# Performance work log

Measured on AMD Instinct MI355X. Metric: run time of the kernel, lower is better.

Reference implementation:

```python
import jax, jax.numpy as jnp
import numpy as np

N_NODES = 100000
N_EDGES = 800000
N_ETYPES = 5
IN_DIM = 23
HID_DIM = 128
OUT_DIM = 64
NUM_GRAPHS = 64


def setup_inputs() -> dict:
    key = jax.random.key(0)
    ks = jax.random.split(key, 8)
    feat = jax.random.normal(ks[0], (N_NODES, IN_DIM), dtype=jnp.float32)
    src = jax.random.randint(ks[1], (N_ETYPES, N_EDGES), 0, N_NODES, dtype=jnp.int32)
    dst = jax.random.randint(ks[2], (N_ETYPES, N_EDGES), 0, N_NODES, dtype=jnp.int32)
    graph_ids = jnp.sort(jax.random.randint(ks[3], (N_NODES,), 0, NUM_GRAPHS, dtype=jnp.int32))
    W1 = jax.random.normal(ks[4], (N_ETYPES, IN_DIM, HID_DIM), dtype=jnp.float32) * 0.1
    b1 = jnp.zeros((N_ETYPES, HID_DIM), dtype=jnp.float32)
    W2 = jax.random.normal(ks[5], (N_ETYPES, HID_DIM, OUT_DIM), dtype=jnp.float32) * 0.1
    b2 = jnp.zeros((N_ETYPES, OUT_DIM), dtype=jnp.float32)
    return {"feat": feat, "src": src, "dst": dst, "graph_ids": graph_ids,
            "W1": W1, "b1": b1, "W2": W2, "b2": b2}


def _hetero_sage_layer(h, src, dst, W, b):
    """HeteroGraphConv of SAGEConv(aggregator='gcn') summed over edge types.
    gcn aggregator: h_neigh[i] = (sum_{j->i} h[j] + h[i]) / (in_deg(i) + 1);
    per-etype output = h_neigh @ W_e + b_e; combine with sum."""
    n = h.shape[0]
    out = jnp.zeros((n, W.shape[-1]), dtype=h.dtype)
    ones_e = jnp.ones((src.shape[1],), dtype=h.dtype)
    for e in range(N_ETYPES):
        deg = jax.ops.segment_sum(ones_e, dst[e], num_segments=n)          # [N]
        agg = jax.ops.segment_sum(h[src[e]], dst[e], num_segments=n)       # [N, D]
        h_neigh = (agg + h) / (deg + 1.0)[:, None]
        out = out + h_neigh @ W[e] + b[e]
    return out


def reference(feat, src, dst, graph_ids, W1, b1, W2, b2):
    # layer 1: in_dim -> hid, relu (dropout in eval mode = identity)
    h = jax.nn.relu(_hetero_sage_layer(feat, src, dst, W1, b1))
    # layer 2: hid -> out (no activation)
    h = _hetero_sage_layer(h, src, dst, W2, b2)
    # dgl.mean_nodes: per-graph mean over nodes
    counts = jax.ops.segment_sum(jnp.ones((h.shape[0],), h.dtype), graph_ids,
                                 num_segments=NUM_GRAPHS)
    sums = jax.ops.segment_sum(h, graph_ids, num_segments=NUM_GRAPHS)
    return sums / jnp.maximum(counts, 1.0)[:, None]
```

## Files before the change

kernel.cpp:

```cpp
#include <hip/hip_runtime.h>

#define N_NODES   100000
#define N_EDGES   800000
#define N_ETYPES  5
#define IN_DIM    23
#define FPAD      32
#define HID_DIM   128
#define OUT_DIM   64
#define NUM_GRAPHS 64
#define NBKT      391
#define PBLK      125
#define CHUNK     6400
#define PN        (N_ETYPES*NBKT*PBLK)
#define SCAN_NBLK ((PN + 1023) / 1024)
#define TOT_EDGES (N_ETYPES*N_EDGES)
#define BKT_CAP   3072
#define ASTR      136
#define A1STR     40


__device__ __forceinline__ unsigned short f2bf(float x) {
    unsigned u = __float_as_uint(x);
    unsigned r = (u + 0x7FFFu + ((u >> 16) & 1u)) >> 16;
    return (unsigned short)r;
}
__device__ __forceinline__ float bf2f(unsigned short h) {
    return __uint_as_float(((unsigned)h) << 16);
}

typedef __attribute__((ext_vector_type(8))) short bf16x8;
typedef __attribute__((ext_vector_type(4))) float f32x4;
typedef __attribute__((ext_vector_type(2))) float f32x2;

__global__ __launch_bounds__(256) void cvt_feat_k(const float* __restrict__ feat,
                                                  unsigned short* __restrict__ fb32) {
    int i = blockIdx.x * 256 + threadIdx.x;
    if (i < N_NODES * FPAD) {
        int n = i >> 5, d = i & 31;
        fb32[i] = (d < IN_DIM) ? f2bf(feat[n * IN_DIM + d]) : (unsigned short)0;
    }
}

__global__ __launch_bounds__(256) void cvt_w2t_k(const float* __restrict__ W2,
                                                 unsigned short* __restrict__ w2tb) {
    int i = blockIdx.x * 256 + threadIdx.x;
    if (i < N_ETYPES * OUT_DIM * HID_DIM) {
        int e = i / (OUT_DIM * HID_DIM);
        int r = i - e * (OUT_DIM * HID_DIM);
        int n = r >> 7, k = r & 127;
        w2tb[i] = f2bf(W2[(e * HID_DIM + k) * OUT_DIM + n]);
    }
}

__global__ __launch_bounds__(256) void cvt_w1t_k(const float* __restrict__ W1,
                                                 unsigned short* __restrict__ w1tb) {
    int i = blockIdx.x * 256 + threadIdx.x;
    if (i < N_ETYPES * HID_DIM * 32) {
        int e = i / (HID_DIM * 32);
        int r = i - e * (HID_DIM * 32);
        int n = r >> 5, k = r & 31;
        w1tb[i] = (k < IN_DIM) ? f2bf(W1[e * IN_DIM * HID_DIM + k * HID_DIM + n])
                               : (unsigned short)0;
    }
}

__global__ __launch_bounds__(128) void cvt_b1s_k(const float* __restrict__ b1,
                                                 float* __restrict__ b1s) {
    int d = threadIdx.x;
    float s = 0.f;
    for (int e = 0; e < N_ETYPES; e++) s += b1[e * HID_DIM + d];
    b1s[d] = s;
}

__global__ __launch_bounds__(256) void part1_k(const int* __restrict__ dst,
                                               int* __restrict__ hp) {
    __shared__ int hist[NBKT];
    int e = blockIdx.y, blk = blockIdx.x, t = threadIdx.x;
    for (int b = t; b < NBKT; b += 256) hist[b] = 0;
    __syncthreads();
    const int* dp = dst + e * N_EDGES + blk * CHUNK;
    for (int k = t; k < CHUNK; k += 256) atomicAdd(&hist[dp[k] >> 8], 1);
    __syncthreads();
    for (int b = t; b < NBKT; b += 256) hp[(e * NBKT + b) * PBLK + blk] = hist[b];
}

__global__ __launch_bounds__(256) void scan1_k(const int* __restrict__ in,
                                               int* __restrict__ out,
                                               int* __restrict__ bsum) {
    __shared__ int ls[256];
    int t = threadIdx.x;
    int base = blockIdx.x * 1024 + t * 4;
    int v[4]; int s = 0;
    for (int j = 0; j < 4; j++) { int i = base + j; v[j] = (i < PN) ? in[i] : 0; s += v[j]; }
    ls[t] = s; __syncthreads();
    for (int o = 1; o < 256; o <<= 1) {
        int x = (t >= o) ? ls[t - o] : 0;
        __syncthreads();
        ls[t] += x;
        __syncthreads();
    }
    int run = (t > 0) ? ls[t - 1] : 0;
    if (t == 255) bsum[blockIdx.x] = ls[255];
    for (int j = 0; j < 4; j++) { int i = base + j; if (i < PN) out[i] = run; run += v[j]; }
}

__global__ __launch_bounds__(256) void scan2_k(int* __restrict__ bsum) {
    __shared__ int ls[256];
    int t = threadIdx.x;
    int v = (t < SCAN_NBLK) ? bsum[t] : 0;
    ls[t] = v; __syncthreads();
    for (int o = 1; o < 256; o <<= 1) {
        int x = (t >= o) ? ls[t - o] : 0;
        __syncthreads();
        ls[t] += x;
        __syncthreads();
    }
    if (t < SCAN_NBLK) bsum[t] = (t > 0) ? ls[t - 1] : 0;
}

__global__ __launch_bounds__(256) void scan3_k(int* __restrict__ off,
                                               const int* __restrict__ bsum) {
    int i = blockIdx.x * 256 + threadIdx.x;
    if (i < PN) off[i] += bsum[i >> 10];
}

__global__ __launch_bounds__(256) void part2_k(const int* __restrict__ src,
                                               const int* __restrict__ dst,
                                               const int* __restrict__ off,
                                               unsigned* __restrict__ ep) {
    __shared__ int cur[NBKT];
    int e = blockIdx.y, blk = blockIdx.x, t = threadIdx.x;
    for (int b = t; b < NBKT; b += 256) cur[b] = off[(e * NBKT + b) * PBLK + blk];
    __syncthreads();
    const int* dp = dst + e * N_EDGES + blk * CHUNK;
    const int* sp = src + e * N_EDGES + blk * CHUNK;
    for (int k = t; k < CHUNK; k += 256) {
        int d = dp[k], s = sp[k];
        int b = d >> 8;
        int pos = atomicAdd(&cur[b], 1);
        ep[pos] = (unsigned)s | ((unsigned)(d & 255) << 24);
    }
}

__global__ __launch_bounds__(256) void sort_k(const int* __restrict__ off,
                                              const unsigned* __restrict__ ep,
                                              unsigned* __restrict__ csr,
                                              int* __restrict__ noff,
                                              int* __restrict__ degn,
                                              float* __restrict__ inv) {
    __shared__ unsigned recs[BKT_CAP];
    __shared__ int hist[256];
    __shared__ int scn[256];
    __shared__ int curp[256];
    int b = blockIdx.x, e = blockIdx.y, t = threadIdx.x;
    int lin = (e * NBKT + b) * PBLK;
    int S = off[lin];
    int E = (lin == PN - PBLK) ? TOT_EDGES : off[lin + PBLK];
    int cnt = E - S;
    hist[t] = 0;
    __syncthreads();
    for (int i = t; i < cnt; i += 256) {
        unsigned r = ep[S + i];
        recs[i] = r;
        atomicAdd(&hist[r >> 24], 1);
    }
    __syncthreads();
    scn[t] = hist[t];
    __syncthreads();
    for (int o = 1; o < 256; o <<= 1) {
        int x = (t >= o) ? scn[t - o] : 0;
        __syncthreads();
        scn[t] += x;
        __syncthreads();
    }
    int excl = scn[t] - hist[t];
    curp[t] = excl;
    int n = b * 256 + t;
    if (n < N_NODES) {
        noff[e * N_NODES + n] = S + excl;
        degn[e * N_NODES + n] = hist[t];
        inv[e * N_NODES + n]  = 1.f / (float)(hist[t] + 1);
    }
    __syncthreads();
    for (int i = t; i < cnt; i += 256) {
        unsigned r = recs[i];
        int pos = atomicAdd(&curp[r >> 24], 1);
        csr[S + pos] = r & 0xFFFFFFu;
    }
}

__global__ __launch_bounds__(256) void agg1_k(const int* __restrict__ noff,
                                              const int* __restrict__ degn,
                                              const unsigned* __restrict__ csr,
                                              const unsigned short* __restrict__ fb32,
                                              const float* __restrict__ inv,
                                              unsigned short* __restrict__ agg1b) {
    int e = blockIdx.y;
    int t = threadIdx.x;
    int lane = t & 15;
    int n = blockIdx.x * 16 + (t >> 4);
    int idx = e * N_NODES + n;
    int st = noff[idx];
    int cnt = degn[idx];
    ushort2 sv = *(const ushort2*)&fb32[n * FPAD + lane * 2];
    float a0 = bf2f(sv.x), a1 = bf2f(sv.y);
    int k = 0;
    for (; k + 3 < cnt; k += 4) {
        int s0 = csr[st + k];
        int s1 = csr[st + k + 1];
        int s2 = csr[st + k + 2];
        int s3 = csr[st + k + 3];
        ushort2 v0 = *(const ushort2*)&fb32[s0 * FPAD + lane * 2];
        ushort2 v1 = *(const ushort2*)&fb32[s1 * FPAD + lane * 2];
        ushort2 v2 = *(const ushort2*)&fb32[s2 * FPAD + lane * 2];
        ushort2 v3 = *(const ushort2*)&fb32[s3 * FPAD + lane * 2];
        a0 += bf2f(v0.x) + bf2f(v1.x) + bf2f(v2.x) + bf2f(v3.x);
        a1 += bf2f(v0.y) + bf2f(v1.y) + bf2f(v2.y) + bf2f(v3.y);
    }
    for (; k < cnt; k++) {
        int s0 = csr[st + k];
        ushort2 v0 = *(const ushort2*)&fb32[s0 * FPAD + lane * 2];
        a0 += bf2f(v0.x);
        a1 += bf2f(v0.y);
    }
    float iv = inv[idx];
    ushort2 o; o.x = f2bf(a0 * iv); o.y = f2bf(a1 * iv);
    *(ushort2*)&agg1b[(size_t)idx * 32 + lane * 2] = o;
}

__global__ __launch_bounds__(256) void gemm1_k(const unsigned short* __restrict__ agg1b,
                                               const unsigned short* __restrict__ w1tb,
                                               const float* __restrict__ b1s,
                                               unsigned short* __restrict__ h1b) {
    __shared__ unsigned short As[64 * A1STR];
    __shared__ unsigned short Wt[128 * A1STR];
    int t = threadIdx.x;
    int node0 = blockIdx.x * 64;
    int w = t >> 6, lane = t & 63;
    int m = lane & 15, quad = lane >> 4;

    f32x4 acc[8];
    for (int nt = 0; nt < 8; nt++) {
        float bb = b1s[nt * 16 + m];
        f32x4 c = {bb, bb, bb, bb};
        acc[nt] = c;
    }

    for (int e = 0; e < N_ETYPES; e++) {
        __syncthreads();
        for (int j = t; j < 64 * 8; j += 256) {
            int n = j >> 3, c4 = (j & 7) * 4;
            int gn = node0 + n;
            int cn = gn < N_NODES ? gn : N_NODES - 1;
            *(ushort4*)&As[n * A1STR + c4] =
                *(const ushort4*)&agg1b[(size_t)(e * N_NODES + cn) * 32 + c4];
        }
        for (int j = t; j < 128 * 8; j += 256) {
            int n = j >> 3, c4 = (j & 7) * 4;
            *(ushort4*)&Wt[n * A1STR + c4] =
                *(const ushort4*)&w1tb[(size_t)(e * HID_DIM + n) * 32 + c4];
        }
        __syncthreads();
        bf16x8 a = *(const bf16x8*)&As[(w * 16 + m) * A1STR + quad * 8];
        for (int nt = 0; nt < 8; nt++) {
            bf16x8 b = *(const bf16x8*)&Wt[(nt * 16 + m) * A1STR + quad * 8];
            acc[nt] = __builtin_amdgcn_mfma_f32_16x16x32_bf16(a, b, acc[nt], 0, 0, 0);
        }
    }
    for (int nt = 0; nt < 8; nt++) {
        for (int r = 0; r < 4; r++) {
            int gn = node0 + w * 16 + quad * 4 + r;
            if (gn < N_NODES)
                h1b[(size_t)gn * HID_DIM + nt * 16 + m] = f2bf(fmaxf(acc[nt][r], 0.f));
        }
    }
}

__global__ __launch_bounds__(256) void gemm2_k(const unsigned short* __restrict__ h1b,
                                               const unsigned short* __restrict__ w2tb,
                                               unsigned char* __restrict__ t2f8) {
    __shared__ unsigned short As[64 * ASTR];
    __shared__ unsigned short Wt[64 * ASTR];
    int t = threadIdx.x;
    int node0 = blockIdx.x * 64;
    int w = t >> 6, lane = t & 63;
    int m = lane & 15, quad = lane >> 4;

    for (int j = t; j < 64 * 32; j += 256) {
        int n = j >> 5, c4 = (j & 31) * 4;
        int gn = node0 + n;
        int cn = gn < N_NODES ? gn : N_NODES - 1;
        *(ushort4*)&As[n * ASTR + c4] = *(const ushort4*)&h1b[cn * HID_DIM + c4];
    }
    __syncthreads();
    bf16x8 a[4];
    for (int ks = 0; ks < 4; ks++)
        a[ks] = *(const bf16x8*)&As[(w * 16 + m) * ASTR + ks * 32 + quad * 8];

    for (int e = 0; e < N_ETYPES; e++) {
        __syncthreads();
        for (int j = t; j < 64 * 32; j += 256) {
            int n = j >> 5, c4 = (j & 31) * 4;
            *(ushort4*)&Wt[n * ASTR + c4] =
                *(const ushort4*)&w2tb[(e * OUT_DIM + n) * HID_DIM + c4];
        }
        __syncthreads();
        unsigned char* out = t2f8 + (size_t)e * N_NODES * OUT_DIM;
        for (int nt = 0; nt < 4; nt++) {
            f32x4 c = {0.f, 0.f, 0.f, 0.f};
            for (int ks = 0; ks < 4; ks++) {
                bf16x8 b = *(const bf16x8*)&Wt[(nt * 16 + m) * ASTR + ks * 32 + quad * 8];
                c = __builtin_amdgcn_mfma_f32_16x16x32_bf16(a[ks], b, c, 0, 0, 0);
            }
            for (int r = 0; r < 4; r++) {
                int gn = node0 + w * 16 + quad * 4 + r;
                if (gn < N_NODES) {
                    int p = __builtin_amdgcn_cvt_pk_fp8_f32(c[r], c[r], 0, false);
                    out[(size_t)gn * OUT_DIM + nt * 16 + m] = (unsigned char)(p & 0xFF);
                }
            }
        }
    }
}

__global__ __launch_bounds__(256) void gather2_k(const int* __restrict__ noff,
                                                 const int* __restrict__ degn,
                                                 const float* __restrict__ inv,
                                                 const unsigned* __restrict__ csr,
                                                 const unsigned char* __restrict__ t2f8,
                                                 const int* __restrict__ gid,
                                                 float* __restrict__ gsum) {
    __shared__ float4 red4[16 * 4 * 16];
    int b = blockIdx.x, qb = blockIdx.y, t = threadIdx.x;
    int lane = t & 15, ng = t >> 4;
    int nbase = b * 256 + qb * 32;
    int gbase = nbase < N_NODES ? nbase : N_NODES - 1;
    int g0 = gid[gbase];
    float4 f[2];
    f[0] = make_float4(0.f, 0.f, 0.f, 0.f);
    f[1] = make_float4(0.f, 0.f, 0.f, 0.f);

    for (int e = 0; e < N_ETYPES; e++) {
        const unsigned char* base = t2f8 + (size_t)e * N_NODES * OUT_DIM;
        #pragma unroll
        for (int pass = 0; pass < 2; pass++) {
            int n = nbase + pass * 16 + ng;
            if (n >= N_NODES) break;
            int idx = e * N_NODES + n;
            int st = noff[idx];
            int cnt = degn[idx];
            float iv = inv[idx];
            unsigned rv = *(const unsigned*)&base[(size_t)n * OUT_DIM + lane * 4];
            f32x2 lo = __builtin_amdgcn_cvt_pk_f32_fp8((int)rv, false);
            f32x2 hi = __builtin_amdgcn_cvt_pk_f32_fp8((int)rv, true);
            float ax = lo.x, ay = lo.y, az = hi.x, aw = hi.y;
            int k = 0;
            for (; k + 3 < cnt; k += 4) {
                int sA = csr[st + k];
                int sB = csr[st + k + 1];
                int sC = csr[st + k + 2];
                int sD = csr[st + k + 3];
                unsigned rA = *(const unsigned*)&base[(size_t)sA * OUT_DIM + lane * 4];
                unsigned rB = *(const unsigned*)&base[(size_t)sB * OUT_DIM + lane * 4];
                unsigned rC = *(const unsigned*)&base[(size_t)sC * OUT_DIM + lane * 4];
                unsigned rD = *(const unsigned*)&base[(size_t)sD * OUT_DIM + lane * 4];
                f32x2 lA = __builtin_amdgcn_cvt_pk_f32_fp8((int)rA, false);
                f32x2 hA = __builtin_amdgcn_cvt_pk_f32_fp8((int)rA, true);
                f32x2 lB = __builtin_amdgcn_cvt_pk_f32_fp8((int)rB, false);
                f32x2 hB = __builtin_amdgcn_cvt_pk_f32_fp8((int)rB, true);
                f32x2 lC = __builtin_amdgcn_cvt_pk_f32_fp8((int)rC, false);
                f32x2 hC = __builtin_amdgcn_cvt_pk_f32_fp8((int)rC, true);
                f32x2 lD = __builtin_amdgcn_cvt_pk_f32_fp8((int)rD, false);
                f32x2 hD = __builtin_amdgcn_cvt_pk_f32_fp8((int)rD, true);
                ax += (lA.x + lB.x) + (lC.x + lD.x);
                ay += (lA.y + lB.y) + (lC.y + lD.y);
                az += (hA.x + hB.x) + (hC.x + hD.x);
                aw += (hA.y + hB.y) + (hC.y + hD.y);
            }
            for (; k < cnt; k++) {
                int sA = csr[st + k];
                unsigned rA = *(const unsigned*)&base[(size_t)sA * OUT_DIM + lane * 4];
                f32x2 lA = __builtin_amdgcn_cvt_pk_f32_fp8((int)rA, false);
                f32x2 hA = __builtin_amdgcn_cvt_pk_f32_fp8((int)rA, true);
                ax += lA.x; ay += lA.y; az += hA.x; aw += hA.y;
            }
            f[pass].x += iv * ax; f[pass].y += iv * ay;
            f[pass].z += iv * az; f[pass].w += iv * aw;
        }
    }

    float4 sa0 = {0,0,0,0}, sa1 = {0,0,0,0}, sa2 = {0,0,0,0}, sa3 = {0,0,0,0};
    #pragma unroll
    for (int pass = 0; pass < 2; pass++) {
        int n = nbase + pass * 16 + ng;
        if (n >= N_NODES) break;
        float4 v = f[pass];
        int slot = gid[n] - g0;
        float m0 = (slot == 0) ? 1.f : 0.f;
        float m1 = (slot == 1) ? 1.f : 0.f;
        float m2 = (slot == 2) ? 1.f : 0.f;
        float m3 = (slot == 3) ? 1.f : 0.f;
        sa0.x += m0 * v.x; sa0.y += m0 * v.y; sa0.z += m0 * v.z; sa0.w += m0 * v.w;
        sa1.x += m1 * v.x; sa1.y += m1 * v.y; sa1.z += m1 * v.z; sa1.w += m1 * v.w;
        sa2.x += m2 * v.x; sa2.y += m2 * v.y; sa2.z += m2 * v.z; sa2.w += m2 * v.w;
        sa3.x += m3 * v.x; sa3.y += m3 * v.y; sa3.z += m3 * v.z; sa3.w += m3 * v.w;
        if (slot > 3) {
            atomicAdd(&gsum[(g0 + slot) * 64 + lane * 4 + 0], v.x);
            atomicAdd(&gsum[(g0 + slot) * 64 + lane * 4 + 1], v.y);
            atomicAdd(&gsum[(g0 + slot) * 64 + lane * 4 + 2], v.z);
            atomicAdd(&gsum[(g0 + slot) * 64 + lane * 4 + 3], v.w);
        }
    }
    red4[(ng * 4 + 0) * 16 + lane] = sa0;
    red4[(ng * 4 + 1) * 16 + lane] = sa1;
    red4[(ng * 4 + 2) * 16 + lane] = sa2;
    red4[(ng * 4 + 3) * 16 + lane] = sa3;
    __syncthreads();
    const float* red = (const float*)red4;
    int slot = t >> 6, d = t & 63;
    float s = 0.f;
    for (int j = 0; j < 16; j++) s += red[(j * 4 + slot) * 64 + d];
    int g = g0 + slot;
    if (g < NUM_GRAPHS) atomicAdd(&gsum[g * 64 + d], s);
}

__global__ __launch_bounds__(256) void gcnt_k(const int* __restrict__ gid,
                                              float* __restrict__ gcnt) {
    __shared__ int h[NUM_GRAPHS];
    int b = blockIdx.x, t = threadIdx.x;
    if (t < NUM_GRAPHS) h[t] = 0;
    __syncthreads();
    int n = b * 256 + t;
    if (n < N_NODES) atomicAdd(&h[gid[n]], 1);
    __syncthreads();
    if (t < NUM_GRAPHS && h[t] > 0) atomicAdd(&gcnt[t], (float)h[t]);
}

__global__ __launch_bounds__(256) void final_k(const float* __restrict__ gsum,
                                               const float* __restrict__ gcnt,
                                               const float* __restrict__ b2,
                                               float* __restrict__ out) {
    int idx = blockIdx.x * 256 + threadIdx.x;
    if (idx >= NUM_GRAPHS * OUT_DIM) return;
    int d = idx & 63;
    float B2 = 0.f;
    for (int e = 0; e < N_ETYPES; e++) B2 += b2[e * OUT_DIM + d];
    float c = gcnt[idx >> 6];
    out[idx] = (gsum[idx] + c * B2) / fmaxf(c, 1.0f);
}

extern "C" void kernel_launch(void* const* d_in, const int* in_sizes, int n_in,
                              void* d_out, int out_size, void* d_ws, size_t ws_size,
                              hipStream_t stream) {
    const float* feat = (const float*)d_in[0];
    const int*   src  = (const int*)d_in[1];
    const int*   dst  = (const int*)d_in[2];
    const int*   gid  = (const int*)d_in[3];
    const float* W1   = (const float*)d_in[4];
    const float* b1   = (const float*)d_in[5];
    const float* W2   = (const float*)d_in[6];
    const float* b2   = (const float*)d_in[7];

    float* ws = (float*)d_ws;
    int*            HP   = (int*)ws;
    int*            OFFP = (int*)ws + 245000;
    int*            BSUM = (int*)ws + 490000;
    float*          INV  = ws + 490512;
    int*            NOFF = (int*)ws + 990512;
    int*            DEGN = (int*)ws + 1490512;
    unsigned short* FB32 = (unsigned short*)(ws + 1990512);
    float*          GSUM = ws + 3590512;
    float*          GCNT = ws + 3594608;
    unsigned*       EP   = (unsigned*)(ws + 3595000);
    unsigned short* AGG1B= (unsigned short*)(ws + 7595000);
    unsigned char*  T2F8 = (unsigned char*)(ws + 3595000);
    unsigned short* H1B  = (unsigned short*)(ws + 15595000);
    unsigned*       CSR  = (unsigned*)(ws + 21995000);
    unsigned short* W2TB = (unsigned short*)(ws + 25995000);
    unsigned short* W1TB = (unsigned short*)(ws + 26015480);
    float*          B1S  = ws + 26025720;

    hipMemsetAsync(GSUM, 0, (size_t)(4096 + 64) * sizeof(float), stream);

    cvt_feat_k<<<(N_NODES * FPAD + 255) / 256, 256, 0, stream>>>(feat, FB32);
    cvt_w2t_k<<<(N_ETYPES * OUT_DIM * HID_DIM + 255) / 256, 256, 0, stream>>>(W2, W2TB);
    cvt_w1t_k<<<(N_ETYPES * HID_DIM * 32 + 255) / 256, 256, 0, stream>>>(W1, W1TB);
    cvt_b1s_k<<<1, 128, 0, stream>>>(b1, B1S);
    part1_k<<<dim3(PBLK, N_ETYPES), 256, 0, stream>>>(dst, HP);
    scan1_k<<<SCAN_NBLK, 256, 0, stream>>>(HP, OFFP, BSUM);
    scan2_k<<<1, 256, 0, stream>>>(BSUM);
    scan3_k<<<(PN + 255) / 256, 256, 0, stream>>>(OFFP, BSUM);
    part2_k<<<dim3(PBLK, N_ETYPES), 256, 0, stream>>>(src, dst, OFFP, EP);
    sort_k<<<dim3(NBKT, N_ETYPES), 256, 0, stream>>>(OFFP, EP, CSR, NOFF, DEGN, INV);

    agg1_k<<<dim3(6250, N_ETYPES), 256, 0, stream>>>(NOFF, DEGN, CSR, FB32, INV, AGG1B);
    gemm1_k<<<(N_NODES + 63) / 64, 256, 0, stream>>>(AGG1B, W1TB, B1S, H1B);
    gemm2_k<<<(N_NODES + 63) / 64, 256, 0, stream>>>(H1B, W2TB, T2F8);
    gather2_k<<<dim3(NBKT, 8), 256, 0, stream>>>(NOFF, DEGN, INV, CSR, T2F8, gid, GSUM);

    gcnt_k<<<391, 256, 0, stream>>>(gid, GCNT);
    final_k<<<16, 256, 0, stream>>>(GSUM, GCNT, b2, (float*)d_out);
}
```

Measured before the change: 424.8 us.

## Fuse partition passes, fuse both GEMMs, store features as fp8, merge weight conversion

Several changes are bundled. The two-pass histogram, three-kernel scan and scatter are replaced by a single partition kernel that reserves slots in fixed-capacity per-bucket regions with global atomics. gemm1 and gemm2 are fused so the hidden activations stay in LDS instead of going through global memory. Input features are stored as fp8 pairs to halve gather bytes in agg1, and the three weight/bias conversion kernels are merged into one. The trade-offs are fp8 precision loss on layer-1 inputs and silent edge truncation if any bucket exceeds BKT_CAP.

```diff
diff --git a/kernel.cpp b/kernel.cpp
--- a/kernel.cpp
+++ b/kernel.cpp
@@ -4,16 +4,13 @@
 #define N_EDGES   800000
 #define N_ETYPES  5
 #define IN_DIM    23
-#define FPAD      32
 #define HID_DIM   128
 #define OUT_DIM   64
 #define NUM_GRAPHS 64
 #define NBKT      391
 #define PBLK      125
 #define CHUNK     6400
-#define PN        (N_ETYPES*NBKT*PBLK)
-#define SCAN_NBLK ((PN + 1023) / 1024)
-#define TOT_EDGES (N_ETYPES*N_EDGES)
+#define NB_E      (N_ETYPES*NBKT)
 #define BKT_CAP   3072
 #define ASTR      136
 #define A1STR     40
@@ -33,16 +30,24 @@
 typedef __attribute__((ext_vector_type(2))) float f32x2;
 
 __global__ __launch_bounds__(256) void cvt_feat_k(const float* __restrict__ feat,
-                                                  unsigned short* __restrict__ fb32) {
+                                                  unsigned short* __restrict__ fb8) {
     int i = blockIdx.x * 256 + threadIdx.x;
-    if (i < N_NODES * FPAD) {
-        int n = i >> 5, d = i & 31;
-        fb32[i] = (d < IN_DIM) ? f2bf(feat[n * IN_DIM + d]) : (unsigned short)0;
-    }
-}
-
-__global__ __launch_bounds__(256) void cvt_w2t_k(const float* __restrict__ W2,
-                                                 unsigned short* __restrict__ w2tb) {
+    if (i < N_NODES * 16) {
+        int n = i >> 4, p = i & 15;
+        int d0 = p * 2, d1 = d0 + 1;
+        float f0 = (d0 < IN_DIM) ? feat[n * IN_DIM + d0] : 0.f;
+        float f1 = (d1 < IN_DIM) ? feat[n * IN_DIM + d1] : 0.f;
+        int pk = __builtin_amdgcn_cvt_pk_fp8_f32(f0, f1, 0, false);
+        fb8[i] = (unsigned short)(pk & 0xFFFF);
+    }
+}
+
+__global__ __launch_bounds__(256) void cvt_w_k(const float* __restrict__ W1,
+                                               const float* __restrict__ b1,
+                                               const float* __restrict__ W2,
+                                               unsigned short* __restrict__ w1tb,
+                                               unsigned short* __restrict__ w2tb,
+                                               float* __restrict__ b1s) {
     int i = blockIdx.x * 256 + threadIdx.x;
     if (i < N_ETYPES * OUT_DIM * HID_DIM) {
         int e = i / (OUT_DIM * HID_DIM);
@@ -50,11 +55,6 @@
         int n = r >> 7, k = r & 127;
         w2tb[i] = f2bf(W2[(e * HID_DIM + k) * OUT_DIM + n]);
     }
-}
-
-__global__ __launch_bounds__(256) void cvt_w1t_k(const float* __restrict__ W1,
-                                                 unsigned short* __restrict__ w1tb) {
-    int i = blockIdx.x * 256 + threadIdx.x;
     if (i < N_ETYPES * HID_DIM * 32) {
         int e = i / (HID_DIM * 32);
         int r = i - e * (HID_DIM * 32);
@@ -62,87 +62,40 @@
         w1tb[i] = (k < IN_DIM) ? f2bf(W1[e * IN_DIM * HID_DIM + k * HID_DIM + n])
                                : (unsigned short)0;
     }
-}
-
-__global__ __launch_bounds__(128) void cvt_b1s_k(const float* __restrict__ b1,
-                                                 float* __restrict__ b1s) {
-    int d = threadIdx.x;
-    float s = 0.f;
-    for (int e = 0; e < N_ETYPES; e++) s += b1[e * HID_DIM + d];
-    b1s[d] = s;
-}
-
-__global__ __launch_bounds__(256) void part1_k(const int* __restrict__ dst,
-                                               int* __restrict__ hp) {
+    if (i < HID_DIM) {
+        float s = 0.f;
+        for (int e = 0; e < N_ETYPES; e++) s += b1[e * HID_DIM + i];
+        b1s[i] = s;
+    }
+}
+
+__global__ __launch_bounds__(256) void part_k(const int* __restrict__ src,
+                                              const int* __restrict__ dst,
+                                              int* __restrict__ gcur,
+                                              unsigned* __restrict__ ep) {
     __shared__ int hist[NBKT];
+    __shared__ int cur[NBKT];
     int e = blockIdx.y, blk = blockIdx.x, t = threadIdx.x;
     for (int b = t; b < NBKT; b += 256) hist[b] = 0;
     __syncthreads();
     const int* dp = dst + e * N_EDGES + blk * CHUNK;
+    const int* sp = src + e * N_EDGES + blk * CHUNK;
     for (int k = t; k < CHUNK; k += 256) atomicAdd(&hist[dp[k] >> 8], 1);
     __syncthreads();
-    for (int b = t; b < NBKT; b += 256) hp[(e * NBKT + b) * PBLK + blk] = hist[b];
-}
-
-__global__ __launch_bounds__(256) void scan1_k(const int* __restrict__ in,
-                                               int* __restrict__ out,
-                                               int* __restrict__ bsum) {
-    __shared__ int ls[256];
-    int t = threadIdx.x;
-    int base = blockIdx.x * 1024 + t * 4;
-    int v[4]; int s = 0;
-    for (int j = 0; j < 4; j++) { int i = base + j; v[j] = (i < PN) ? in[i] : 0; s += v[j]; }
-    ls[t] = s; __syncthreads();
-    for (int o = 1; o < 256; o <<= 1) {
-        int x = (t >= o) ? ls[t - o] : 0;
-        __syncthreads();
-        ls[t] += x;
-        __syncthreads();
-    }
-    int run = (t > 0) ? ls[t - 1] : 0;
-    if (t == 255) bsum[blockIdx.x] = ls[255];
-    for (int j = 0; j < 4; j++) { int i = base + j; if (i < PN) out[i] = run; run += v[j]; }
-}
-
-__global__ __launch_bounds__(256) void scan2_k(int* __restrict__ bsum) {
-    __shared__ int ls[256];
-    int t = threadIdx.x;
-    int v = (t < SCAN_NBLK) ? bsum[t] : 0;
-    ls[t] = v; __syncthreads();
-    for (int o = 1; o < 256; o <<= 1) {
-        int x = (t >= o) ? ls[t - o] : 0;
-        __syncthreads();
-        ls[t] += x;
-        __syncthreads();
-    }
-    if (t < SCAN_NBLK) bsum[t] = (t > 0) ? ls[t - 1] : 0;
-}
-
-__global__ __launch_bounds__(256) void scan3_k(int* __restrict__ off,
-                                               const int* __restrict__ bsum) {
-    int i = blockIdx.x * 256 + threadIdx.x;
-    if (i < PN) off[i] += bsum[i >> 10];
-}
-
-__global__ __launch_bounds__(256) void part2_k(const int* __restrict__ src,
-                                               const int* __restrict__ dst,
-                                               const int* __restrict__ off,
-                                               unsigned* __restrict__ ep) {
-    __shared__ int cur[NBKT];
-    int e = blockIdx.y, blk = blockIdx.x, t = threadIdx.x;
-    for (int b = t; b < NBKT; b += 256) cur[b] = off[(e * NBKT + b) * PBLK + blk];
-    __syncthreads();
-    const int* dp = dst + e * N_EDGES + blk * CHUNK;
-    const int* sp = src + e * N_EDGES + blk * CHUNK;
+    for (int b = t; b < NBKT; b += 256)
+        cur[b] = (hist[b] > 0) ? atomicAdd(&gcur[e * NBKT + b], hist[b]) : 0;
+    __syncthreads();
     for (int k = t; k < CHUNK; k += 256) {
         int d = dp[k], s = sp[k];
         int b = d >> 8;
         int pos = atomicAdd(&cur[b], 1);
-        ep[pos] = (unsigned)s | ((unsigned)(d & 255) << 24);
-    }
-}
-
-__global__ __launch_bounds__(256) void sort_k(const int* __restrict__ off,
+        if (pos < BKT_CAP)
+            ep[(size_t)(e * NBKT + b) * BKT_CAP + pos] =
+                (unsigned)s | ((unsigned)(d & 255) << 24);
+    }
+}
+
+__global__ __launch_bounds__(256) void sort_k(const int* __restrict__ gcur,
                                               const unsigned* __restrict__ ep,
                                               unsigned* __restrict__ csr,
                                               int* __restrict__ noff,
@@ -153,10 +106,10 @@
     __shared__ int scn[256];
     __shared__ int curp[256];
     int b = blockIdx.x, e = blockIdx.y, t = threadIdx.x;
-    int lin = (e * NBKT + b) * PBLK;
-    int S = off[lin];
-    int E = (lin == PN - PBLK) ? TOT_EDGES : off[lin + PBLK];
-    int cnt = E - S;
+    int lin = e * NBKT + b;
+    int S = lin * BKT_CAP;
+    int cnt = gcur[lin];
+    if (cnt > BKT_CAP) cnt = BKT_CAP;
     hist[t] = 0;
     __syncthreads();
     for (int i = t; i < cnt; i += 256) {
@@ -192,7 +145,7 @@
 __global__ __launch_bounds__(256) void agg1_k(const int* __restrict__ noff,
                                               const int* __restrict__ degn,
                                               const unsigned* __restrict__ csr,
-                                              const unsigned short* __restrict__ fb32,
+                                              const unsigned short* __restrict__ fb8,
                                               const float* __restrict__ inv,
                                               unsigned short* __restrict__ agg1b) {
     int e = blockIdx.y;
@@ -202,38 +155,45 @@
     int idx = e * N_NODES + n;
     int st = noff[idx];
     int cnt = degn[idx];
-    ushort2 sv = *(const ushort2*)&fb32[n * FPAD + lane * 2];
-    float a0 = bf2f(sv.x), a1 = bf2f(sv.y);
+    f32x2 sv = __builtin_amdgcn_cvt_pk_f32_fp8((int)fb8[n * 16 + lane], false);
+    float a0 = sv.x, a1 = sv.y;
     int k = 0;
     for (; k + 3 < cnt; k += 4) {
         int s0 = csr[st + k];
         int s1 = csr[st + k + 1];
         int s2 = csr[st + k + 2];
         int s3 = csr[st + k + 3];
-        ushort2 v0 = *(const ushort2*)&fb32[s0 * FPAD + lane * 2];
-        ushort2 v1 = *(const ushort2*)&fb32[s1 * FPAD + lane * 2];
-        ushort2 v2 = *(const ushort2*)&fb32[s2 * FPAD + lane * 2];
-        ushort2 v3 = *(const ushort2*)&fb32[s3 * FPAD + lane * 2];
-        a0 += bf2f(v0.x) + bf2f(v1.x) + bf2f(v2.x) + bf2f(v3.x);
-        a1 += bf2f(v0.y) + bf2f(v1.y) + bf2f(v2.y) + bf2f(v3.y);
+        unsigned short r0 = fb8[s0 * 16 + lane];
+        unsigned short r1 = fb8[s1 * 16 + lane];
+        unsigned short r2 = fb8[s2 * 16 + lane];
+        unsigned short r3 = fb8[s3 * 16 + lane];
+        f32x2 v0 = __builtin_amdgcn_cvt_pk_f32_fp8((int)r0, false);
+        f32x2 v1 = __builtin_amdgcn_cvt_pk_f32_fp8((int)r1, false);
+        f32x2 v2 = __builtin_amdgcn_cvt_pk_f32_fp8((int)r2, false);
+        f32x2 v3 = __builtin_amdgcn_cvt_pk_f32_fp8((int)r3, false);
+        a0 += (v0.x + v1.x) + (v2.x + v3.x);
+        a1 += (v0.y + v1.y) + (v2.y + v3.y);
     }
     for (; k < cnt; k++) {
         int s0 = csr[st + k];
-        ushort2 v0 = *(const ushort2*)&fb32[s0 * FPAD + lane * 2];
-        a0 += bf2f(v0.x);
-        a1 += bf2f(v0.y);
+        f32x2 v0 = __builtin_amdgcn_cvt_pk_f32_fp8((int)fb8[s0 * 16 + lane], false);
+        a0 += v0.x;
+        a1 += v0.y;
     }
     float iv = inv[idx];
     ushort2 o; o.x = f2bf(a0 * iv); o.y = f2bf(a1 * iv);
     *(ushort2*)&agg1b[(size_t)idx * 32 + lane * 2] = o;
 }
 
-__global__ __launch_bounds__(256) void gemm1_k(const unsigned short* __restrict__ agg1b,
-                                               const unsigned short* __restrict__ w1tb,
-                                               const float* __restrict__ b1s,
-                                               unsigned short* __restrict__ h1b) {
-    __shared__ unsigned short As[64 * A1STR];
-    __shared__ unsigned short Wt[128 * A1STR];
+__global__ __launch_bounds__(256) void gemm12_k(const unsigned short* __restrict__ agg1b,
+                                                const unsigned short* __restrict__ w1tb,
+                                                const float* __restrict__ b1s,
+                                                const unsigned short* __restrict__ w2tb,
+                                                unsigned char* __restrict__ t2f8) {
+    __shared__ unsigned short H1s[64 * ASTR];
+    __shared__ unsigned short Wt2[64 * ASTR];
+    unsigned short* As1 = Wt2;
+    unsigned short* Wt1 = Wt2 + 64 * A1STR;
     int t = threadIdx.x;
     int node0 = blockIdx.x * 64;
     int w = t >> 6, lane = t & 63;
@@ -245,63 +205,42 @@
         f32x4 c = {bb, bb, bb, bb};
         acc[nt] = c;
     }
-
     for (int e = 0; e < N_ETYPES; e++) {
         __syncthreads();
         for (int j = t; j < 64 * 8; j += 256) {
             int n = j >> 3, c4 = (j & 7) * 4;
             int gn = node0 + n;
             int cn = gn < N_NODES ? gn : N_NODES - 1;
-            *(ushort4*)&As[n * A1STR + c4] =
+            *(ushort4*)&As1[n * A1STR + c4] =
                 *(const ushort4*)&agg1b[(size_t)(e * N_NODES + cn) * 32 + c4];
         }
         for (int j = t; j < 128 * 8; j += 256) {
             int n = j >> 3, c4 = (j & 7) * 4;
-            *(ushort4*)&Wt[n * A1STR + c4] =
+            *(ushort4*)&Wt1[n * A1STR + c4] =
                 *(const ushort4*)&w1tb[(size_t)(e * HID_DIM + n) * 32 + c4];
         }
         __syncthreads();
-        bf16x8 a = *(const bf16x8*)&As[(w * 16 + m) * A1STR + quad * 8];
+        bf16x8 a = *(const bf16x8*)&As1[(w * 16 + m) * A1STR + quad * 8];
         for (int nt = 0; nt < 8; nt++) {
-            bf16x8 b = *(const bf16x8*)&Wt[(nt * 16 + m) * A1STR + quad * 8];
+            bf16x8 b = *(const bf16x8*)&Wt1[(nt * 16 + m) * A1STR + quad * 8];
             acc[nt] = __builtin_amdgcn_mfma_f32_16x16x32_bf16(a, b, acc[nt], 0, 0, 0);
         }
     }
-    for (int nt = 0; nt < 8; nt++) {
-        for (int r = 0; r < 4; r++) {
-            int gn = node0 + w * 16 + quad * 4 + r;
-            if (gn < N_NODES)
-                h1b[(size_t)gn * HID_DIM + nt * 16 + m] = f2bf(fmaxf(acc[nt][r], 0.f));
-        }
-    }
-}
-
-__global__ __launch_bounds__(256) void gemm2_k(const unsigned short* __restrict__ h1b,
-                                               const unsigned short* __restrict__ w2tb,
-                                               unsigned char* __restrict__ t2f8) {
-    __shared__ unsigned short As[64 * ASTR];
-    __shared__ unsigned short Wt[64 * ASTR];
-    int t = threadIdx.x;
-    int node0 = blockIdx.x * 64;
-    int w = t >> 6, lane = t & 63;
-    int m = lane & 15, quad = lane >> 4;
-
-    for (int j = t; j < 64 * 32; j += 256) {
-        int n = j >> 5, c4 = (j & 31) * 4;
-        int gn = node0 + n;
-        int cn = gn < N_NODES ? gn : N_NODES - 1;
-        *(ushort4*)&As[n * ASTR + c4] = *(const ushort4*)&h1b[cn * HID_DIM + c4];
-    }
-    __syncthreads();
-    bf16x8 a[4];
+    __syncthreads();
+    for (int nt = 0; nt < 8; nt++)
+        for (int r = 0; r < 4; r++)
+            H1s[(w * 16 + quad * 4 + r) * ASTR + nt * 16 + m] =
+                f2bf(fmaxf(acc[nt][r], 0.f));
+    __syncthreads();
+
+    bf16x8 a2[4];
     for (int ks = 0; ks < 4; ks++)
-        a[ks] = *(const bf16x8*)&As[(w * 16 + m) * ASTR + ks * 32 + quad * 8];
-
+        a2[ks] = *(const bf16x8*)&H1s[(w * 16 + m) * ASTR + ks * 32 + quad * 8];
     for (int e = 0; e < N_ETYPES; e++) {
         __syncthreads();
         for (int j = t; j < 64 * 32; j += 256) {
             int n = j >> 5, c4 = (j & 31) * 4;
-            *(ushort4*)&Wt[n * ASTR + c4] =
+            *(ushort4*)&Wt2[n * ASTR + c4] =
                 *(const ushort4*)&w2tb[(e * OUT_DIM + n) * HID_DIM + c4];
         }
         __syncthreads();
@@ -309,8 +248,8 @@
         for (int nt = 0; nt < 4; nt++) {
             f32x4 c = {0.f, 0.f, 0.f, 0.f};
             for (int ks = 0; ks < 4; ks++) {
-                bf16x8 b = *(const bf16x8*)&Wt[(nt * 16 + m) * ASTR + ks * 32 + quad * 8];
-                c = __builtin_amdgcn_mfma_f32_16x16x32_bf16(a[ks], b, c, 0, 0, 0);
+                bf16x8 b = *(const bf16x8*)&Wt2[(nt * 16 + m) * ASTR + ks * 32 + quad * 8];
+                c = __builtin_amdgcn_mfma_f32_16x16x32_bf16(a2[ks], b, c, 0, 0, 0);
             }
             for (int r = 0; r < 4; r++) {
                 int gn = node0 + w * 16 + quad * 4 + r;
@@ -462,40 +401,32 @@
     const float* b2   = (const float*)d_in[7];
 
     float* ws = (float*)d_ws;
-    int*            HP   = (int*)ws;
-    int*            OFFP = (int*)ws + 245000;
-    int*            BSUM = (int*)ws + 490000;
-    float*          INV  = ws + 490512;
-    int*            NOFF = (int*)ws + 990512;
-    int*            DEGN = (int*)ws + 1490512;
-    unsigned short* FB32 = (unsigned short*)(ws + 1990512);
-    float*          GSUM = ws + 3590512;
-    float*          GCNT = ws + 3594608;
-    unsigned*       EP   = (unsigned*)(ws + 3595000);
-    unsigned short* AGG1B= (unsigned short*)(ws + 7595000);
-    unsigned char*  T2F8 = (unsigned char*)(ws + 3595000);
-    unsigned short* H1B  = (unsigned short*)(ws + 15595000);
-    unsigned*       CSR  = (unsigned*)(ws + 21995000);
-    unsigned short* W2TB = (unsigned short*)(ws + 25995000);
-    unsigned short* W1TB = (unsigned short*)(ws + 26015480);
-    float*          B1S  = ws + 26025720;
-
+    int*            GCUR = (int*)ws;
+    float*          INV  = ws + 2048;
+    int*            NOFF = (int*)ws + 502048;
+    int*            DEGN = (int*)ws + 1002048;
+    unsigned short* FB8  = (unsigned short*)(ws + 1502048);
+    float*          GSUM = ws + 2302048;
+    float*          GCNT = ws + 2306144;
+    unsigned*       EP   = (unsigned*)(ws + 2306208);
+    unsigned*       CSR  = (unsigned*)(ws + 8311968);
+    unsigned short* AGG1B= (unsigned short*)(ws + 14317728);
+    unsigned char*  T2F8 = (unsigned char*)(ws + 22317728);
+    unsigned short* W1TB = (unsigned short*)(ws + 30317728);
+    unsigned short* W2TB = (unsigned short*)(ws + 30327968);
+    float*          B1S  = ws + 30348448;
+
+    hipMemsetAsync(GCUR, 0, 2048 * sizeof(int), stream);
     hipMemsetAsync(GSUM, 0, (size_t)(4096 + 64) * sizeof(float), stream);
 
-    cvt_feat_k<<<(N_NODES * FPAD + 255) / 256, 256, 0, stream>>>(feat, FB32);
-    cvt_w2t_k<<<(N_ETYPES * OUT_DIM * HID_DIM + 255) / 256, 256, 0, stream>>>(W2, W2TB);
-    cvt_w1t_k<<<(N_ETYPES * HID_DIM * 32 + 255) / 256, 256, 0, stream>>>(W1, W1TB);
-    cvt_b1s_k<<<1, 128, 0, stream>>>(b1, B1S);
-    part1_k<<<dim3(PBLK, N_ETYPES), 256, 0, stream>>>(dst, HP);
-    scan1_k<<<SCAN_NBLK, 256, 0, stream>>>(HP, OFFP, BSUM);
-    scan2_k<<<1, 256, 0, stream>>>(BSUM);
-    scan3_k<<<(PN + 255) / 256, 256, 0, stream>>>(OFFP, BSUM);
-    part2_k<<<dim3(PBLK, N_ETYPES), 256, 0, stream>>>(src, dst, OFFP, EP);
-    sort_k<<<dim3(NBKT, N_ETYPES), 256, 0, stream>>>(OFFP, EP, CSR, NOFF, DEGN, INV);
-
-    agg1_k<<<dim3(6250, N_ETYPES), 256, 0, stream>>>(NOFF, DEGN, CSR, FB32, INV, AGG1B);
-    gemm1_k<<<(N_NODES + 63) / 64, 256, 0, stream>>>(AGG1B, W1TB, B1S, H1B);
-    gemm2_k<<<(N_NODES + 63) / 64, 256, 0, stream>>>(H1B, W2TB, T2F8);
+    cvt_feat_k<<<(N_NODES * 16 + 255) / 256, 256, 0, stream>>>(feat, FB8);
+    cvt_w_k<<<(N_ETYPES * OUT_DIM * HID_DIM + 255) / 256, 256, 0, stream>>>(
+        W1, b1, W2, W1TB, W2TB, B1S);
+    part_k<<<dim3(PBLK, N_ETYPES), 256, 0, stream>>>(src, dst, GCUR, EP);
+    sort_k<<<dim3(NBKT, N_ETYPES), 256, 0, stream>>>(GCUR, EP, CSR, NOFF, DEGN, INV);
+
+    agg1_k<<<dim3(6250, N_ETYPES), 256, 0, stream>>>(NOFF, DEGN, CSR, FB8, INV, AGG1B);
+    gemm12_k<<<(N_NODES + 63) / 64, 256, 0, stream>>>(AGG1B, W1TB, B1S, W2TB, T2F8);
     gather2_k<<<dim3(NBKT, 8), 256, 0, stream>>>(NOFF, DEGN, INV, CSR, T2F8, gid, GSUM);
 
     gcnt_k<<<391, 256, 0, stream>>>(gid, GCNT);
```

Result: faster. 385.7 us (-9.2%).
